# Kernel optimization log

Hardware: AMD Instinct MI355X
Metric: run time of the kernel (lower is better)

The kernel has to match this reference:

```python
import jax, jax.numpy as jnp
import numpy as np

HIDDEN = 2048
NUM_HEADS = 16
HEAD_DIM = HIDDEN // NUM_HEADS
ROPE_THETA = 10000.0
B, S = 2, 2048
NEG_INF = jnp.finfo(jnp.float32).min


def _rope_tables(seq_len, head_dim, base):
    inv_freq = 1.0 / (base ** (jnp.arange(0, head_dim, 2, dtype=jnp.float32) / head_dim))
    t = jnp.arange(seq_len, dtype=jnp.float32)
    freqs = jnp.outer(t, inv_freq)                 # [S, head_dim/2]
    emb = jnp.concatenate([freqs, freqs], axis=-1) # [S, head_dim]
    return jnp.cos(emb), jnp.sin(emb)


def _rotate_half(x):
    x1, x2 = jnp.split(x, 2, axis=-1)
    return jnp.concatenate([-x2, x1], axis=-1)


def _apply_rope(q, k, cos, sin, position_ids):
    # q,k: [B,H,S,D]; cos/sin: [S_max,D]; position_ids: [B,S]
    c = cos[position_ids][:, None, :, :]  # [B,1,S,D]
    s = sin[position_ids][:, None, :, :]
    q = q * c + _rotate_half(q) * s
    k = k * c + _rotate_half(k) * s
    return q, k


def setup_inputs() -> dict:
    key = jax.random.key(0)
    ks = jax.random.split(key, 5)
    hidden_states = jax.random.normal(ks[0], (B, S, HIDDEN), dtype=jnp.float32)
    # causal additive mask, shape (B,1,S,S)
    causal = jnp.triu(jnp.full((S, S), NEG_INF, dtype=jnp.float32), k=1)
    attention_mask = jnp.broadcast_to(causal[None, None], (B, 1, S, S))
    position_ids = jnp.broadcast_to(jnp.arange(S, dtype=jnp.int32)[None], (B, S))
    scale = 1.0 / np.sqrt(HIDDEN)
    Wq = jax.random.normal(ks[1], (HIDDEN, HIDDEN), dtype=jnp.float32) * scale
    Wk = jax.random.normal(ks[2], (HIDDEN, HIDDEN), dtype=jnp.float32) * scale
    Wv = jax.random.normal(ks[3], (HIDDEN, HIDDEN), dtype=jnp.float32) * scale
    Wo = jax.random.normal(ks[4], (HIDDEN, HIDDEN), dtype=jnp.float32) * scale
    return {"hidden_states": hidden_states, "attention_mask": attention_mask,
            "position_ids": position_ids, "Wq": Wq, "Wk": Wk, "Wv": Wv, "Wo": Wo}


def reference(hidden_states, attention_mask, position_ids, Wq, Wk, Wv, Wo):
    bsz, q_len, _ = hidden_states.shape
    def proj(W):
        # nn.Linear: x @ W.T -> [B,S,H*D] -> [B,H,S,D]
        y = jnp.einsum('bse,fe->bsf', hidden_states, W)
        return y.reshape(bsz, q_len, NUM_HEADS, HEAD_DIM).transpose(0, 2, 1, 3)
    q, k, v = proj(Wq), proj(Wk), proj(Wv)
    cos, sin = _rope_tables(q_len, HEAD_DIM, ROPE_THETA)
    q, k = _apply_rope(q, k, cos, sin, position_ids)
    scores = jnp.einsum('bhqd,bhkd->bhqk', q, k) / np.sqrt(HEAD_DIM)
    scores = scores + attention_mask
    scores = jnp.maximum(scores, NEG_INF)
    weights = jax.nn.softmax(scores.astype(jnp.float32), axis=-1).astype(q.dtype)
    attn = jnp.einsum('bhqk,bhkd->bhqd', weights, v)
    attn = attn.transpose(0, 2, 1, 3).reshape(bsz, q_len, HIDDEN)
    return jnp.einsum('bsf,ef->bse', attn, Wo)
```

## Files before the change

### kernel.cpp

```cpp
#include <hip/hip_runtime.h>
#include <hip/hip_bf16.h>

typedef __attribute__((ext_vector_type(4))) float f32x4;
typedef __attribute__((ext_vector_type(8))) short bf16x8;

__device__ __forceinline__ short f2b(float f) {
  unsigned u = __builtin_bit_cast(unsigned, f);
  u += 0x7FFFu + ((u >> 16) & 1u);
  return (short)(u >> 16);
}
__device__ __forceinline__ float b2f(short s) {
  unsigned u = ((unsigned)(unsigned short)s) << 16;
  return __builtin_bit_cast(float, u);
}

__device__ __forceinline__ void async16(const void* g, void* l) {
  __builtin_amdgcn_global_load_lds(
      (const __attribute__((address_space(1))) void*)g,
      (__attribute__((address_space(3))) void*)l, 16, 0, 0);
}

#define BM 128
#define BN 128
#define BK 64

__global__ __launch_bounds__(256) void cvt_kernel(
    const float* __restrict__ X, const float* __restrict__ Wq,
    const float* __restrict__ Wk, const float* __restrict__ Wv,
    const float* __restrict__ Wo, short* __restrict__ dst) {
  const size_t u = (size_t)blockIdx.x * 256 + threadIdx.x;
  const float* src;
  short* d;
  size_t off;
  if (u < 1048576) {
    src = X; d = dst; off = u * 8;
  } else {
    const size_t j = u - 1048576;
    const int ten = (int)(j >> 19);
    off = (j & 524287) * 8;
    src = (ten == 0) ? Wq : (ten == 1) ? Wk : (ten == 2) ? Wv : Wo;
    d = dst + 8388608 + (size_t)ten * 4194304;
  }
  const f32x4 lo = *(const f32x4*)(src + off);
  const f32x4 hi = *(const f32x4*)(src + off + 4);
  bf16x8 v;
#pragma unroll
  for (int i = 0; i < 4; ++i) { v[i] = f2b(lo[i]); v[i + 4] = f2b(hi[i]); }
  *(bf16x8*)(d + off) = v;
}

template <int MODE>
__global__ __launch_bounds__(256, 2) void gemm_kernel(
    const short* __restrict__ A,
    const short* __restrict__ B0,
    const short* __restrict__ B1,
    const short* __restrict__ B2,
    void* __restrict__ O0,
    short* __restrict__ O1,
    short* __restrict__ O2) {
  constexpr int K = 2048;
  const int m0 = blockIdx.x * BM;
  const int n0 = blockIdx.y * BN;
  const short* B;
  if (MODE == 0) {
    const int wsel = blockIdx.z;
    B = (wsel == 0) ? B0 : ((wsel == 1) ? B1 : B2);
  } else {
    B = B0;
  }

  __shared__ __align__(16) short As[BM * BK];
  __shared__ __align__(16) short Bs[BN * BK];

  const int t = threadIdx.x;
  const int wave = t >> 6;
  const int lane = t & 63;
  const int qd = lane >> 4;
  const int ln = lane & 15;
  const int wr = wave >> 1;
  const int wc = wave & 1;

  const f32x4 zero = {0.f, 0.f, 0.f, 0.f};
  f32x4 acc[4][4];
#pragma unroll
  for (int i = 0; i < 4; ++i)
#pragma unroll
    for (int j = 0; j < 4; ++j) acc[i][j] = zero;

  const int srow = t >> 3;
  const int sgp = (t & 7) ^ (srow & 7);
  const short* Ag = A + (size_t)(m0 + srow) * K + sgp * 8;
  const short* Bg = B + (size_t)(n0 + srow) * K + sgp * 8;
  short* Asw = &As[wave * 512];
  short* Bsw = &Bs[wave * 512];

  for (int k0 = 0; k0 < K; k0 += BK) {
    __syncthreads();
#pragma unroll
    for (int r = 0; r < 4; ++r) {
      async16(Ag + (size_t)(r * 32) * K + k0, Asw + r * 2048);
      async16(Bg + (size_t)(r * 32) * K + k0, Bsw + r * 2048);
    }
    __syncthreads();

    bf16x8 af[2][4], bf[2][4];
#pragma unroll
    for (int kc = 0; kc < 2; ++kc) {
#pragma unroll
      for (int i = 0; i < 4; ++i) {
        const int m = wr * 64 + i * 16 + ln;
        af[kc][i] = *(const bf16x8*)&As[m * BK + (((kc * 4 + qd) ^ (m & 7)) << 3)];
        const int n = wc * 64 + i * 16 + ln;
        bf[kc][i] = *(const bf16x8*)&Bs[n * BK + (((kc * 4 + qd) ^ (n & 7)) << 3)];
      }
    }
#pragma unroll
    for (int kc = 0; kc < 2; ++kc)
#pragma unroll
      for (int i = 0; i < 4; ++i)
#pragma unroll
        for (int j = 0; j < 4; ++j)
          acc[i][j] = __builtin_amdgcn_mfma_f32_16x16x32_bf16(af[kc][i], bf[kc][j],
                                                              acc[i][j], 0, 0, 0);
  }

#pragma unroll
  for (int i = 0; i < 4; ++i) {
#pragma unroll
    for (int j = 0; j < 4; ++j) {
      const int n = n0 + wc * 64 + j * 16 + ln;
#pragma unroll
      for (int rr = 0; rr < 4; ++rr) {
        const int m = m0 + wr * 64 + i * 16 + qd * 4 + rr;
        if (MODE == 1) {
          ((float*)O0)[(size_t)m * 2048 + n] = acc[i][j][rr];
        } else {
          const short v = f2b(acc[i][j][rr]);
          const int b = m >> 11, s = m & 2047;
          const int h = n >> 7, d = n & 127;
          if (blockIdx.z == 0)
            ((short*)O0)[((size_t)(b * 16 + h) * 2048 + s) * 128 + d] = v;
          else if (blockIdx.z == 1)
            O1[((size_t)(b * 16 + h) * 2048 + s) * 128 + d] = v;
          else
            O2[((size_t)(b * 16 + h) * 128 + d) * 2048 + s] = v;
        }
      }
    }
  }
}

__global__ void rope_kernel(short* __restrict__ Q,
                            short* __restrict__ Kb,
                            const int* __restrict__ pos_ids) {
  const int idx = blockIdx.x * 256 + threadIdx.x;
  const int d = idx & 63;
  const int row = idx >> 6;
  const int tsel = row >> 16;
  const int r = row & 65535;
  const int s = r & 2047;
  const int b = r >> 15;
  const int pos = pos_ids[b * 2048 + s];
  const float invf = __builtin_exp2f(-(float)d * 0.20762050593117475f);
  const float ang = (float)pos * invf;
  const float c = cosf(ang), sn = sinf(ang);
  short* P = (tsel ? Kb : Q) + (size_t)r * 128;
  const float x1 = b2f(P[d]);
  const float x2 = b2f(P[d + 64]);
  P[d] = f2b(x1 * c - x2 * sn);
  P[d + 64] = f2b(x2 * c + x1 * sn);
}

__global__ __launch_bounds__(256, 4) void attn_kernel(
    const short* __restrict__ Q,
    const short* __restrict__ Kbuf,
    const short* __restrict__ Vt,
    short* __restrict__ O) {
  const int n = blockIdx.x;
  const int xcd = n & 7;
  const int m_ = n >> 3;
  const int bh = xcd + 8 * (m_ & 3);
  const int x_ = m_ >> 2;
  const int u_ = x_ & 7;
  const int g_ = x_ >> 3;
  const int qt = (g_ == 0) ? 2 * u_
               : (g_ == 1) ? 31 - 2 * u_
               : (g_ == 2) ? 2 * u_ + 1
                           : 30 - 2 * u_;
  const int q0 = qt * 64;
  const size_t hoff = (size_t)bh * 2048 * 128;
  const short* Qh = Q + hoff;
  const short* Kh = Kbuf + hoff;
  const short* Vh = Vt + hoff;

  __shared__ __align__(16) short Ks[2][32 * 128];
  __shared__ __align__(16) short Vs[2][128 * 32];
  __shared__ __align__(16) short Ps[4][16 * 32];

  const int t = threadIdx.x;
  const int wave = t >> 6;
  const int lane = t & 63;
  const int qd = lane >> 4;
  const int ln = lane & 15;
  const int qw0 = q0 + wave * 16;

  bf16x8 qf[4];
  {
    const short* qp = Qh + (size_t)(qw0 + ln) * 128 + qd * 8;
#pragma unroll
    for (int kc = 0; kc < 4; ++kc) qf[kc] = *(const bf16x8*)(qp + kc * 32);
  }

  const f32x4 zero = {0.f, 0.f, 0.f, 0.f};
  f32x4 oacc[8];
#pragma unroll
  for (int dt = 0; dt < 8; ++dt) oacc[dt] = zero;
  f32x4 lacc = zero;
  float mrow[4] = {-1e30f, -1e30f, -1e30f, -1e30f};

  bf16x8 ones;
#pragma unroll
  for (int i = 0; i < 8; ++i) ones[i] = (short)0x3F80;

  const float rscale = 0.08838834764831845f;
  short* pw = &Ps[wave][0];

  const int kr = t >> 4;
  const int gk = (t & 15) ^ (kr & 7);
  const int vr = t >> 2;
  const int gv = (t & 3) ^ (vr & 3) ^ ((vr >> 2) & 3);
  const short* Kg = Kh + (size_t)kr * 128 + gk * 8;
  const short* Vg = Vh + (size_t)vr * 2048 + gv * 8;
  const int wb = wave * 512;

  const int nkv = 2 * qt + 2;

#pragma unroll
  for (int rd = 0; rd < 2; ++rd) {
    async16(Kg + (size_t)(rd * 16) * 128, &Ks[0][rd * 2048 + wb]);
    async16(Vg + (size_t)rd * 131072, &Vs[0][rd * 2048 + wb]);
  }

  int cur = 0;
  for (int kt = 0; kt < nkv; ++kt) {
    const int k0 = kt * 32;
    __syncthreads();
    if (kt + 1 < nkv) {
      const int k1 = k0 + 32;
#pragma unroll
      for (int rd = 0; rd < 2; ++rd) {
        async16(Kg + (size_t)(k1 + rd * 16) * 128, &Ks[cur ^ 1][rd * 2048 + wb]);
        async16(Vg + (size_t)rd * 131072 + k1, &Vs[cur ^ 1][rd * 2048 + wb]);
      }
    }

    if (k0 <= qw0 + 15) {
      const short* Kc = &Ks[cur][0];
      f32x4 sc[2];
#pragma unroll
      for (int j = 0; j < 2; ++j) {
        sc[j] = zero;
        const int krow = j * 16 + ln;
#pragma unroll
        for (int kc = 0; kc < 4; ++kc) {
          const bf16x8 kf =
              *(const bf16x8*)&Kc[krow * 128 + (((kc * 4 + qd) ^ (krow & 7)) << 3)];
          sc[j] = __builtin_amdgcn_mfma_f32_16x16x32_bf16(qf[kc], kf, sc[j], 0, 0, 0);
        }
      }

      float pvv[2][4];
#pragma unroll
      for (int j = 0; j < 2; ++j)
#pragma unroll
        for (int rr = 0; rr < 4; ++rr) pvv[j][rr] = sc[j][rr] * rscale;
      if (k0 + 31 > qw0) {
#pragma unroll
        for (int j = 0; j < 2; ++j) {
          const int kcol = k0 + j * 16 + ln;
#pragma unroll
          for (int rr = 0; rr < 4; ++rr)
            if (kcol > qw0 + qd * 4 + rr) pvv[j][rr] = -1e30f;
        }
      }

      float tmax[4] = {-1e30f, -1e30f, -1e30f, -1e30f};
#pragma unroll
      for (int j = 0; j < 2; ++j)
#pragma unroll
        for (int rr = 0; rr < 4; ++rr) tmax[rr] = fmaxf(tmax[rr], pvv[j][rr]);
#pragma unroll
      for (int off = 8; off >= 1; off >>= 1)
#pragma unroll
        for (int rr = 0; rr < 4; ++rr)
          tmax[rr] = fmaxf(tmax[rr], __shfl_xor(tmax[rr], off, 16));

      bool grow = false;
#pragma unroll
      for (int rr = 0; rr < 4; ++rr) grow = grow || (tmax[rr] > mrow[rr] + 8.f);
      if (__any(grow)) {
#pragma unroll
        for (int rr = 0; rr < 4; ++rr) {
          const float mnew = fmaxf(mrow[rr], tmax[rr]);
          const float al = __expf(mrow[rr] - mnew);
          mrow[rr] = mnew;
          lacc[rr] *= al;
#pragma unroll
          for (int dt = 0; dt < 8; ++dt) oacc[dt][rr] *= al;
        }
      }

#pragma unroll
      for (int j = 0; j < 2; ++j)
#pragma unroll
        for (int rr = 0; rr < 4; ++rr) {
          const int row = qd * 4 + rr;
          const int col = j * 16 + ln;
          pw[row * 32 + ((((col >> 3) ^ (row & 3) ^ ((row >> 2) & 3)) << 3)) +
             (col & 7)] = f2b(__expf(pvv[j][rr] - mrow[rr]));
        }
      const bf16x8 pf =
          *(const bf16x8*)&pw[ln * 32 + (((qd ^ (ln & 3) ^ ((ln >> 2) & 3)) << 3))];

      const short* Vc = &Vs[cur][0];
#pragma unroll
      for (int dt = 0; dt < 8; ++dt) {
        const int d = dt * 16 + ln;
        const bf16x8 vf =
            *(const bf16x8*)&Vc[d * 32 + (((qd ^ (d & 3) ^ ((d >> 2) & 3)) << 3))];
        oacc[dt] = __builtin_amdgcn_mfma_f32_16x16x32_bf16(pf, vf, oacc[dt], 0, 0, 0);
      }
      lacc = __builtin_amdgcn_mfma_f32_16x16x32_bf16(pf, ones, lacc, 0, 0, 0);
    }
    cur ^= 1;
  }

  const int b = bh >> 4;
  const int h = bh & 15;
  float rl[4];
#pragma unroll
  for (int rr = 0; rr < 4; ++rr) rl[rr] = 1.0f / lacc[rr];
#pragma unroll
  for (int dt = 0; dt < 8; ++dt) {
    const int d = dt * 16 + ln;
#pragma unroll
    for (int rr = 0; rr < 4; ++rr) {
      const int q = qw0 + qd * 4 + rr;
      O[((size_t)(b * 2048 + q)) * 2048 + h * 128 + d] = f2b(oacc[dt][rr] * rl[rr]);
    }
  }
}

extern "C" void kernel_launch(void* const* d_in, const int* in_sizes, int n_in,
                              void* d_out, int out_size, void* d_ws, size_t ws_size,
                              hipStream_t stream) {
  const float* X  = (const float*)d_in[0];
  const int* pos  = (const int*)d_in[2];
  const float* Wq = (const float*)d_in[3];
  const float* Wk = (const float*)d_in[4];
  const float* Wv = (const float*)d_in[5];
  const float* Wo = (const float*)d_in[6];
  float* out = (float*)d_out;

  short* ws = (short*)d_ws;
  short* Xb  = ws;
  short* Wqb = ws + 8388608;
  short* Wkb = Wqb + 4194304;
  short* Wvb = Wkb + 4194304;
  short* Wob = Wvb + 4194304;
  short* Qb  = Wob + 4194304;
  short* Kb  = Qb + 8388608;
  short* Vt  = Kb + 8388608;
  short* Ob  = Vt + 8388608;

  cvt_kernel<<<dim3(12288), 256, 0, stream>>>(X, Wq, Wk, Wv, Wo, Xb);
  gemm_kernel<0><<<dim3(32, 16, 3), 256, 0, stream>>>(Xb, Wqb, Wkb, Wvb,
                                                      Qb, Kb, Vt);
  rope_kernel<<<dim3(32768), 256, 0, stream>>>(Qb, Kb, pos);
  attn_kernel<<<dim3(1024), 256, 0, stream>>>(Qb, Kb, Vt, Ob);
  gemm_kernel<1><<<dim3(32, 16, 1), 256, 0, stream>>>(Ob, Wob, nullptr, nullptr,
                                                      out, nullptr, nullptr);
}
```

Measured before the change: 422.8 us.

## Transpose score MFMA, fold scale into Q, keep P in registers

The QK^T MFMA operands are swapped so each lane owns one query row. The softmax scale and log2(e) are folded into Q during the RoPE pass so exp2 can be used directly. P is packed to bf16 with v_cvt_pk_bf16_f32 and redistributed through lane shuffles instead of a shared-memory round trip, and the row sum is computed with shuffles instead of an extra MFMA against a ones vector. Launch bounds occupancy goes from 4 to 5, which removes LDS traffic and per-row reductions but adds shuffle work and register pressure.

```diff
diff --git a/kernel.cpp b/kernel.cpp
--- a/kernel.cpp
+++ b/kernel.cpp
@@ -3,6 +3,7 @@
 
 typedef __attribute__((ext_vector_type(4))) float f32x4;
 typedef __attribute__((ext_vector_type(8))) short bf16x8;
+typedef __attribute__((ext_vector_type(4))) unsigned u32x4;
 
 __device__ __forceinline__ short f2b(float f) {
   unsigned u = __builtin_bit_cast(unsigned, f);
@@ -12,6 +13,11 @@
 __device__ __forceinline__ float b2f(short s) {
   unsigned u = ((unsigned)(unsigned short)s) << 16;
   return __builtin_bit_cast(float, u);
+}
+__device__ __forceinline__ unsigned cvtpk(float lo, float hi) {
+  unsigned r;
+  asm("v_cvt_pk_bf16_f32 %0, %1, %2" : "=v"(r) : "v"(lo), "v"(hi));
+  return r;
 }
 
 __device__ __forceinline__ void async16(const void* g, void* l) {
@@ -164,14 +170,15 @@
   const float invf = __builtin_exp2f(-(float)d * 0.20762050593117475f);
   const float ang = (float)pos * invf;
   const float c = cosf(ang), sn = sinf(ang);
+  const float qs = tsel ? 1.0f : 0.12751743f;
   short* P = (tsel ? Kb : Q) + (size_t)r * 128;
   const float x1 = b2f(P[d]);
   const float x2 = b2f(P[d + 64]);
-  P[d] = f2b(x1 * c - x2 * sn);
-  P[d + 64] = f2b(x2 * c + x1 * sn);
-}
-
-__global__ __launch_bounds__(256, 4) void attn_kernel(
+  P[d] = f2b((x1 * c - x2 * sn) * qs);
+  P[d + 64] = f2b((x2 * c + x1 * sn) * qs);
+}
+
+__global__ __launch_bounds__(256, 5) void attn_kernel(
     const short* __restrict__ Q,
     const short* __restrict__ Kbuf,
     const short* __restrict__ Vt,
@@ -195,7 +202,6 @@
 
   __shared__ __align__(16) short Ks[2][32 * 128];
   __shared__ __align__(16) short Vs[2][128 * 32];
-  __shared__ __align__(16) short Ps[4][16 * 32];
 
   const int t = threadIdx.x;
   const int wave = t >> 6;
@@ -215,15 +221,8 @@
   f32x4 oacc[8];
 #pragma unroll
   for (int dt = 0; dt < 8; ++dt) oacc[dt] = zero;
-  f32x4 lacc = zero;
-  float mrow[4] = {-1e30f, -1e30f, -1e30f, -1e30f};
-
-  bf16x8 ones;
-#pragma unroll
-  for (int i = 0; i < 8; ++i) ones[i] = (short)0x3F80;
-
-  const float rscale = 0.08838834764831845f;
-  short* pw = &Ps[wave][0];
+  float mrow = -1e30f;
+  float lrow = 0.f;
 
   const int kr = t >> 4;
   const int gk = (t & 15) ^ (kr & 7);
@@ -265,7 +264,7 @@
         for (int kc = 0; kc < 4; ++kc) {
           const bf16x8 kf =
               *(const bf16x8*)&Kc[krow * 128 + (((kc * 4 + qd) ^ (krow & 7)) << 3)];
-          sc[j] = __builtin_amdgcn_mfma_f32_16x16x32_bf16(qf[kc], kf, sc[j], 0, 0, 0);
+          sc[j] = __builtin_amdgcn_mfma_f32_16x16x32_bf16(kf, qf[kc], sc[j], 0, 0, 0);
         }
       }
 
@@ -273,54 +272,68 @@
 #pragma unroll
       for (int j = 0; j < 2; ++j)
 #pragma unroll
-        for (int rr = 0; rr < 4; ++rr) pvv[j][rr] = sc[j][rr] * rscale;
+        for (int rr = 0; rr < 4; ++rr) pvv[j][rr] = sc[j][rr];
       if (k0 + 31 > qw0) {
-#pragma unroll
-        for (int j = 0; j < 2; ++j) {
-          const int kcol = k0 + j * 16 + ln;
+        const int qrow = qw0 + ln;
+#pragma unroll
+        for (int j = 0; j < 2; ++j)
 #pragma unroll
           for (int rr = 0; rr < 4; ++rr)
-            if (kcol > qw0 + qd * 4 + rr) pvv[j][rr] = -1e30f;
+            if (k0 + j * 16 + qd * 4 + rr > qrow) pvv[j][rr] = -1e30f;
+      }
+
+      float tmax = pvv[0][0];
+#pragma unroll
+      for (int j = 0; j < 2; ++j)
+#pragma unroll
+        for (int rr = 0; rr < 4; ++rr) tmax = fmaxf(tmax, pvv[j][rr]);
+      tmax = fmaxf(tmax, __shfl_xor(tmax, 16));
+      tmax = fmaxf(tmax, __shfl_xor(tmax, 32));
+
+      if (__any(tmax > mrow + 8.f)) {
+        const float mnew = fmaxf(mrow, tmax);
+        const float al = __builtin_exp2f(mrow - mnew);
+        mrow = mnew;
+        lrow *= al;
+        float a[4];
+#pragma unroll
+        for (int rr = 0; rr < 4; ++rr) a[rr] = __shfl(al, qd * 4 + rr);
+#pragma unroll
+        for (int dt = 0; dt < 8; ++dt)
+#pragma unroll
+          for (int rr = 0; rr < 4; ++rr) oacc[dt][rr] *= a[rr];
+      }
+
+      float ps = 0.f;
+#pragma unroll
+      for (int j = 0; j < 2; ++j)
+#pragma unroll
+        for (int rr = 0; rr < 4; ++rr) {
+          const float p = __builtin_exp2f(pvv[j][rr] - mrow);
+          pvv[j][rr] = p;
+          ps += p;
         }
-      }
-
-      float tmax[4] = {-1e30f, -1e30f, -1e30f, -1e30f};
-#pragma unroll
-      for (int j = 0; j < 2; ++j)
-#pragma unroll
-        for (int rr = 0; rr < 4; ++rr) tmax[rr] = fmaxf(tmax[rr], pvv[j][rr]);
-#pragma unroll
-      for (int off = 8; off >= 1; off >>= 1)
-#pragma unroll
-        for (int rr = 0; rr < 4; ++rr)
-          tmax[rr] = fmaxf(tmax[rr], __shfl_xor(tmax[rr], off, 16));
-
-      bool grow = false;
-#pragma unroll
-      for (int rr = 0; rr < 4; ++rr) grow = grow || (tmax[rr] > mrow[rr] + 8.f);
-      if (__any(grow)) {
-#pragma unroll
-        for (int rr = 0; rr < 4; ++rr) {
-          const float mnew = fmaxf(mrow[rr], tmax[rr]);
-          const float al = __expf(mrow[rr] - mnew);
-          mrow[rr] = mnew;
-          lacc[rr] *= al;
-#pragma unroll
-          for (int dt = 0; dt < 8; ++dt) oacc[dt][rr] *= al;
-        }
-      }
-
-#pragma unroll
-      for (int j = 0; j < 2; ++j)
-#pragma unroll
-        for (int rr = 0; rr < 4; ++rr) {
-          const int row = qd * 4 + rr;
-          const int col = j * 16 + ln;
-          pw[row * 32 + ((((col >> 3) ^ (row & 3) ^ ((row >> 2) & 3)) << 3)) +
-             (col & 7)] = f2b(__expf(pvv[j][rr] - mrow[rr]));
-        }
-      const bf16x8 pf =
-          *(const bf16x8*)&pw[ln * 32 + (((qd ^ (ln & 3) ^ ((ln >> 2) & 3)) << 3))];
+      ps += __shfl_xor(ps, 16);
+      ps += __shfl_xor(ps, 32);
+      lrow += ps;
+
+      const unsigned A0 = cvtpk(pvv[0][0], pvv[0][1]);
+      const unsigned A1 = cvtpk(pvv[0][2], pvv[0][3]);
+      const unsigned B0 = cvtpk(pvv[1][0], pvv[1][1]);
+      const unsigned B1 = cvtpk(pvv[1][2], pvv[1][3]);
+      const int s0 = ln + ((qd & 1) << 5);
+      const int s1 = s0 + 16;
+      const unsigned a0 = __shfl(A0, s0), a1 = __shfl(A1, s0);
+      const unsigned a2 = __shfl(A0, s1), a3 = __shfl(A1, s1);
+      const unsigned b0 = __shfl(B0, s0), b1 = __shfl(B1, s0);
+      const unsigned b2 = __shfl(B0, s1), b3 = __shfl(B1, s1);
+      const bool useA = (qd < 2);
+      u32x4 pr;
+      pr[0] = useA ? a0 : b0;
+      pr[1] = useA ? a1 : b1;
+      pr[2] = useA ? a2 : b2;
+      pr[3] = useA ? a3 : b3;
+      const bf16x8 pf = __builtin_bit_cast(bf16x8, pr);
 
       const short* Vc = &Vs[cur][0];
 #pragma unroll
@@ -330,7 +343,6 @@
             *(const bf16x8*)&Vc[d * 32 + (((qd ^ (d & 3) ^ ((d >> 2) & 3)) << 3))];
         oacc[dt] = __builtin_amdgcn_mfma_f32_16x16x32_bf16(pf, vf, oacc[dt], 0, 0, 0);
       }
-      lacc = __builtin_amdgcn_mfma_f32_16x16x32_bf16(pf, ones, lacc, 0, 0, 0);
     }
     cur ^= 1;
   }
@@ -339,7 +351,7 @@
   const int h = bh & 15;
   float rl[4];
 #pragma unroll
-  for (int rr = 0; rr < 4; ++rr) rl[rr] = 1.0f / lacc[rr];
+  for (int rr = 0; rr < 4; ++rr) rl[rr] = 1.0f / __shfl(lrow, qd * 4 + rr);
 #pragma unroll
   for (int dt = 0; dt < 8; ++dt) {
     const int d = dt * 16 + ln;
```

After: 428.7 us. Within noise of the previous version (+1.4%).
